# Kernel optimization log

Measured on AMD Instinct MI355X. Metric: run time of the kernel, lower is better.

The kernel has to match this reference:

```python
import jax, jax.numpy as jnp
import numpy as np

SQRT5 = 2.2360679774997896


def setup_inputs() -> dict:
    key = jax.random.key(0)
    k1, k2, k3 = jax.random.split(key, 3)
    n, m, d = 1024, 1024, 8
    X1 = jax.random.normal(k1, (n, d), dtype=jnp.float32)
    X2 = jax.random.normal(k2, (m, d), dtype=jnp.float32)
    c = jnp.asarray(1.0, dtype=jnp.float32)  # overall_scaling (scalar param)
    # character_length: positive lengthscales per feature
    l = 0.5 + jax.random.uniform(k3, (d,), dtype=jnp.float32)
    return {"X1": X1, "X2": X2, "c": c, "l": l}


def reference(X1, X2, c, l):
    # X1: [n, d], X2: [m, d] -> out [n, d, m, d]
    d = l.shape[0]
    inv_l2 = 1.0 / (l * l)                       # [d]
    DX1X2 = X1[:, None, :] - X2[None, :, :]      # [n, m, d]
    # scaled pairwise distance r[i,j] = || (X1_i - X2_j) / l ||
    r = jnp.sqrt(jnp.sum((DX1X2 / l) ** 2, axis=-1))   # [n, m]
    fr = (5.0 / 3.0) * jnp.exp(-SQRT5 * r)             # [n, m]
    # M[a,b] = (1/l^2) * eye(d) with column-wise broadcast (matches torch):
    M = inv_l2 * jnp.eye(d, dtype=l.dtype)             # [d, d], diag = 1/l^2
    A = fr * (1.0 + SQRT5 * r)                         # [n, m]
    D = DX1X2 * inv_l2                                 # [n, m, d]
    # k[i,a,j,b] = A[i,j]*M[a,b] - 5*fr[i,j]*D[i,j,a]*D[i,j,b]
    k = jnp.einsum('ij,ab->iajb', A, M) - 5.0 * jnp.einsum('ij,ija,ijb->iajb', fr, D, D)
    return (c * c) * k
```

## Files before the change

### kernel.cpp

```cpp
#include <hip/hip_runtime.h>

#define SQRT5F 2.2360679774997896f


__global__ __launch_bounds__(512) void deriv2_matern52_kernel(
    const float* __restrict__ X1,
    const float* __restrict__ X2,
    const float* __restrict__ c_ptr,
    const float* __restrict__ l_ptr,
    float* __restrict__ out,
    int m )
{
    const int t    = threadIdx.x;
    const int w    = t >> 6;
    const int lane = t & 63;
    const int p    = lane >> 1;
    const int h    = lane & 1;
    const int b0   = h << 2;

    const int i = blockIdx.x;

    const float c  = c_ptr[0];
    const float c2 = c * c;

    float inv_l2[8];
#pragma unroll
    for (int k = 0; k < 8; ++k) {
        const float lv = l_ptr[k];
        inv_l2[k] = 1.0f / (lv * lv);
    }

    float asel[8];
#pragma unroll
    for (int a = 0; a < 8; ++a) asel[a] = (a == w) ? 1.0f : 0.0f;

    float il_w = 0.0f;
#pragma unroll
    for (int a = 0; a < 8; ++a) il_w = fmaf(asel[a], inv_l2[a], il_w);

    float dk[4];
#pragma unroll
    for (int k = 0; k < 4; ++k)
        dk[k] = (((w & 3) == k) && ((w >> 2) == h)) ? 1.0f : 0.0f;

    const float4 x1a = ((const float4*)(X1 + (size_t)i * 8))[0];
    const float4 x1b = ((const float4*)(X1 + (size_t)i * 8))[1];
    const float x1v[8] = { x1a.x, x1a.y, x1a.z, x1a.w,
                           x1b.x, x1b.y, x1b.z, x1b.w };

    float* op = out + (size_t)i * (size_t)(8 * m * 8)
                    + (size_t)w * (size_t)(m * 8)
                    + (size_t)p * 8 + b0;
    const float* xp = X2 + (size_t)p * 8;

    for (int s = 0; s < m; s += 32) {
        const float4 x2a = ((const float4*)xp)[0];
        const float4 x2b = ((const float4*)xp)[1];
        const float x2v[8] = { x2a.x, x2a.y, x2a.z, x2a.w,
                               x2b.x, x2b.y, x2b.z, x2b.w };

        float D[8];
        float r2 = 0.0f;
#pragma unroll
        for (int k = 0; k < 8; ++k) {
            const float dx = x1v[k] - x2v[k];
            D[k] = dx * inv_l2[k];
            r2 += dx * D[k];
        }

        const float r  = sqrtf(r2);
        const float fr = (5.0f / 3.0f) * expf(-SQRT5F * r);
        const float A  = fr * (1.0f + SQRT5F * r);

        const float Acil = A * c2 * il_w;
        const float cf   = -5.0f * fr * c2;

        float Dw = 0.0f;
#pragma unroll
        for (int a = 0; a < 8; ++a) Dw = fmaf(asel[a], D[a], Dw);
        const float Dca = cf * Dw;

        const float Db[4] = { D[b0 + 0], D[b0 + 1], D[b0 + 2], D[b0 + 3] };

        float v[4];
#pragma unroll
        for (int k = 0; k < 4; ++k)
            v[k] = fmaf(dk[k], Acil, Dca * Db[k]);

        *(float4*)op = make_float4(v[0], v[1], v[2], v[3]);

        op += 32 * 8;
        xp += 32 * 8;
    }
}

extern "C" void kernel_launch(void* const* d_in, const int* in_sizes, int n_in,
                              void* d_out, int out_size, void* d_ws, size_t ws_size,
                              hipStream_t stream) {
    const float* X1 = (const float*)d_in[0];
    const float* X2 = (const float*)d_in[1];
    const float* c  = (const float*)d_in[2];
    const float* l  = (const float*)d_in[3];
    float* out = (float*)d_out;

    const int d = in_sizes[3];
    const int n = in_sizes[0] / d;
    const int m = in_sizes[1] / d;

    dim3 grid(n);
    dim3 block(512);
    deriv2_matern52_kernel<<<grid, block, 0, stream>>>(X1, X2, c, l, out, m);
}
```

Measured before the change: 274.4 us.

## Split work across blocks per (i,a) row with 256-thread blocks

Measured after the change: 269.8 us. No clear change (-1.7%).

```diff
diff --git a/kernel.cpp b/kernel.cpp
--- a/kernel.cpp
+++ b/kernel.cpp
@@ -3,7 +3,7 @@
 #define SQRT5F 2.2360679774997896f
 
 
-__global__ __launch_bounds__(512) void deriv2_matern52_kernel(
+__global__ __launch_bounds__(256) void deriv2_matern52_kernel(
     const float* __restrict__ X1,
     const float* __restrict__ X2,
     const float* __restrict__ c_ptr,
@@ -11,14 +11,13 @@
     float* __restrict__ out,
     int m )
 {
-    const int t    = threadIdx.x;
-    const int w    = t >> 6;
-    const int lane = t & 63;
-    const int p    = lane >> 1;
-    const int h    = lane & 1;
-    const int b0   = h << 2;
+    const int t  = threadIdx.x;
+    const int h  = t & 1;
+    const int p  = t >> 1;
 
-    const int i = blockIdx.x;
+    const int bid = blockIdx.x;
+    const int a   = bid & 7;
+    const int i   = bid >> 3;
 
     const float c  = c_ptr[0];
     const float c2 = c * c;
@@ -32,28 +31,26 @@
 
     float asel[8];
 #pragma unroll
-    for (int a = 0; a < 8; ++a) asel[a] = (a == w) ? 1.0f : 0.0f;
+    for (int k = 0; k < 8; ++k) asel[k] = (k == a) ? 1.0f : 0.0f;
 
-    float il_w = 0.0f;
+    float il_a = 0.0f;
 #pragma unroll
-    for (int a = 0; a < 8; ++a) il_w = fmaf(asel[a], inv_l2[a], il_w);
+    for (int k = 0; k < 8; ++k) il_a = fmaf(asel[k], inv_l2[k], il_a);
 
     float dk[4];
 #pragma unroll
     for (int k = 0; k < 4; ++k)
-        dk[k] = (((w & 3) == k) && ((w >> 2) == h)) ? 1.0f : 0.0f;
+        dk[k] = (((a & 3) == k) && ((a >> 2) == h)) ? 1.0f : 0.0f;
 
     const float4 x1a = ((const float4*)(X1 + (size_t)i * 8))[0];
     const float4 x1b = ((const float4*)(X1 + (size_t)i * 8))[1];
     const float x1v[8] = { x1a.x, x1a.y, x1a.z, x1a.w,
                            x1b.x, x1b.y, x1b.z, x1b.w };
 
-    float* op = out + (size_t)i * (size_t)(8 * m * 8)
-                    + (size_t)w * (size_t)(m * 8)
-                    + (size_t)p * 8 + b0;
+    float* op = out + (size_t)bid * (size_t)m * 8 + (size_t)t * 4;
     const float* xp = X2 + (size_t)p * 8;
 
-    for (int s = 0; s < m; s += 32) {
+    for (int s = 0; s < m; s += 128) {
         const float4 x2a = ((const float4*)xp)[0];
         const float4 x2b = ((const float4*)xp)[1];
         const float x2v[8] = { x2a.x, x2a.y, x2a.z, x2a.w,
@@ -72,25 +69,25 @@
         const float fr = (5.0f / 3.0f) * expf(-SQRT5F * r);
         const float A  = fr * (1.0f + SQRT5F * r);
 
-        const float Acil = A * c2 * il_w;
+        const float Acil = A * c2 * il_a;
         const float cf   = -5.0f * fr * c2;
 
-        float Dw = 0.0f;
+        float Da = 0.0f;
 #pragma unroll
-        for (int a = 0; a < 8; ++a) Dw = fmaf(asel[a], D[a], Dw);
-        const float Dca = cf * Dw;
-
-        const float Db[4] = { D[b0 + 0], D[b0 + 1], D[b0 + 2], D[b0 + 3] };
+        for (int k = 0; k < 8; ++k) Da = fmaf(asel[k], D[k], Da);
+        const float Dca = cf * Da;
 
         float v[4];
 #pragma unroll
-        for (int k = 0; k < 4; ++k)
-            v[k] = fmaf(dk[k], Acil, Dca * Db[k]);
+        for (int k = 0; k < 4; ++k) {
+            const float Db = h ? D[4 + k] : D[k];
+            v[k] = fmaf(dk[k], Acil, Dca * Db);
+        }
 
         *(float4*)op = make_float4(v[0], v[1], v[2], v[3]);
 
-        op += 32 * 8;
-        xp += 32 * 8;
+        op += 128 * 8;
+        xp += 128 * 8;
     }
 }
 
@@ -107,7 +104,7 @@
     const int n = in_sizes[0] / d;
     const int m = in_sizes[1] / d;
 
-    dim3 grid(n);
-    dim3 block(512);
+    dim3 grid(n * 8);
+    dim3 block(256);
     deriv2_matern52_kernel<<<grid, block, 0, stream>>>(X1, X2, c, l, out, m);
 }
```
